# Kernel optimization log

Measured on AMD Instinct MI355X. Metric: run time of the kernel, lower is better.

Reference implementation:

```python
import jax, jax.numpy as jnp
import numpy as np

B, C, L = 4, 512, 4096

def setup_inputs() -> dict:
    key = jax.random.key(0)
    k1, k2, k3, k4 = jax.random.split(key, 4)
    proj_query = jax.random.normal(k1, (B, C, L), dtype=jnp.float32)
    proj_key = jax.random.normal(k2, (B, C, L), dtype=jnp.float32)
    proj_val = jax.random.normal(k3, (B, C, L), dtype=jnp.float32)
    # binary padding mask over key positions, broadcast over query axis
    padding_mask = (jax.random.uniform(k4, (B, 1, L)) < 0.9).astype(jnp.float32)
    return {"proj_query": proj_query, "proj_key": proj_key,
            "proj_val": proj_val, "padding_mask": padding_mask}

def reference(proj_query, proj_key, proj_val, padding_mask):
    c = proj_query.shape[1]
    # energy[b,i,j] = sum_c Q[b,c,i] * K[b,c,j]  -> (B, L1, L2)
    energy = jnp.einsum('bci,bcj->bij', proj_query, proj_key)
    attention = energy / jnp.sqrt(jnp.asarray(c, dtype=energy.dtype))
    attention = attention + jnp.log(padding_mask + 1e-6)
    attention = jax.nn.softmax(attention, axis=-1)
    attention = attention * padding_mask
    attention = attention.transpose(0, 2, 1)  # (B, L2, L1)
    out = jnp.einsum('bcj,bji->bci', proj_val, attention)  # (B, C, L1)
    return out, attention
```

## Files before the change

kernel.cpp:

```cpp
#include <hip/hip_runtime.h>

#define B_ 4
#define C_ 512
#define L_ 4096

typedef __attribute__((ext_vector_type(8))) short bf16x8;
typedef __attribute__((ext_vector_type(4))) float f32x4;

#define MFMA16(a, b, c) __builtin_amdgcn_mfma_f32_16x16x32_bf16(a, b, c, 0, 0, 0)

static __device__ __forceinline__ unsigned short f2bf_rne(float f) {
  unsigned u = __float_as_uint(f);
  u += 0x7FFFu + ((u >> 16) & 1u);
  return (unsigned short)(u >> 16);
}
static __device__ __forceinline__ unsigned pack_rne(float a, float b) {
  return (unsigned)f2bf_rne(a) | ((unsigned)f2bf_rne(b) << 16);
}
static __device__ __forceinline__ float bflo2f(unsigned w) {
  return __uint_as_float(w << 16);
}
static __device__ __forceinline__ float bfhi2f(unsigned w) {
  return __uint_as_float(w & 0xFFFF0000u);
}

static __device__ __forceinline__ void g2lds16(const unsigned short* g,
                                               unsigned short* l) {
  __builtin_amdgcn_global_load_lds(
      (const __attribute__((address_space(1))) unsigned int*)g,
      (__attribute__((address_space(3))) unsigned int*)l, 16, 0, 0);
}

#define BAR_() __builtin_amdgcn_s_barrier()
#define LGKM0_() asm volatile("s_waitcnt lgkmcnt(0)" ::: "memory")
#define VMW_(N) asm volatile("s_waitcnt vmcnt(" #N ")" ::: "memory")

__global__ __launch_bounds__(256) void prep_k(
    const float* __restrict__ Q, const float* __restrict__ K,
    const float* __restrict__ V, const float* __restrict__ mask,
    unsigned short* __restrict__ Qt, unsigned short* __restrict__ Kt,
    unsigned short* __restrict__ Vb) {
  int zb = blockIdx.z;
  int t = threadIdx.x;
  __shared__ float tile[64][65];
  if (zb < 8) {
    int b = zb >> 1;
    const float* src = ((zb & 1) ? K : Q) + (size_t)b * C_ * L_;
    unsigned short* dst = ((zb & 1) ? Kt : Qt) + (size_t)b * L_ * C_;
    int i0 = blockIdx.x * 64, c0 = blockIdx.y * 64;
    int cr = t >> 2, ig = (t & 3) * 16;
    const float* s = src + (size_t)(c0 + cr) * L_ + i0 + ig;
#pragma unroll
    for (int q = 0; q < 4; ++q) {
      float4 v = *(const float4*)(s + 4 * q);
      tile[cr][ig + 4 * q + 0] = v.x;
      tile[cr][ig + 4 * q + 1] = v.y;
      tile[cr][ig + 4 * q + 2] = v.z;
      tile[cr][ig + 4 * q + 3] = v.w;
    }
    __syncthreads();
    int ir = t >> 2, cg = (t & 3) * 16;
    unsigned wds[8];
#pragma unroll
    for (int k = 0; k < 8; ++k)
      wds[k] = pack_rne(tile[cg + 2 * k][ir], tile[cg + 2 * k + 1][ir]);
    unsigned short* d = dst + (size_t)(i0 + ir) * C_ + c0 + cg;
    uint4 o0, o1;
    o0.x = wds[0]; o0.y = wds[1]; o0.z = wds[2]; o0.w = wds[3];
    o1.x = wds[4]; o1.y = wds[5]; o1.z = wds[6]; o1.w = wds[7];
    *(uint4*)d = o0;
    *(uint4*)(d + 8) = o1;
  } else {
    int b = zb - 8;
    int flat = blockIdx.x + (blockIdx.y << 6);
    size_t base = (size_t)b * C_ * L_ + (size_t)flat * 4096 + (size_t)t * 16;
    int j = (int)(base & (L_ - 1));
    const float* vp = V + base;
    const float* mp = mask + (size_t)b * L_ + j;
#pragma unroll
    for (int g = 0; g < 2; ++g) {
      float4 v0 = *(const float4*)(vp + g * 8);
      float4 v1 = *(const float4*)(vp + g * 8 + 4);
      float4 m0 = *(const float4*)(mp + g * 8);
      float4 m1 = *(const float4*)(mp + g * 8 + 4);
      uint4 o;
      o.x = pack_rne(v0.x * m0.x, v0.y * m0.y);
      o.y = pack_rne(v0.z * m0.z, v0.w * m0.w);
      o.z = pack_rne(v1.x * m1.x, v1.y * m1.y);
      o.w = pack_rne(v1.z * m1.z, v1.w * m1.w);
      *(uint4*)(Vb + base + g * 8) = o;
    }
  }
}

__device__ __forceinline__ void gemm_8phase(
    const unsigned short* __restrict__ Ab,
    const unsigned short* __restrict__ Bb, int lda, int ldb, int Kdim,
    unsigned short* sA, unsigned short* sB, f32x4 (&acc)[8][4]) {
  const int t = threadIdx.x;
  const int lane = t & 63;
  const int quad = lane >> 4;
  const int l15 = lane & 15;
  const int w = t >> 6;
  const int wm = (w & 1) * 128;
  const int wn = (w >> 1) * 64;
  const int et = (t * 8) ^ (((t >> 5) & 1) << 4);
  const int srw = et >> 5;
  const int scl = et & 31;
  const int nt = Kdim >> 6;

  auto stage = [&](int nom, int hh) {
    int st = nom < nt ? nom : nt - 1;
    int db = nom & 1;
    int h = hh & 1;
    const unsigned short* g;
    unsigned short* l;
    if (hh < 2) {
      g = Bb + (size_t)(h * 128 + srw) * ldb + st * 64 + scl;
      l = sB + db * 16384 + h * 4096 + t * 8;
    } else {
      g = Ab + (size_t)(h * 128 + srw) * lda + st * 64 + scl;
      l = sA + db * 16384 + h * 4096 + t * 8;
    }
    g2lds16(g, l);
    g2lds16(g + 32, l + 8192);
  };
  auto rd = [&](const unsigned short* s, int db, int kc, int row) -> bf16x8 {
    int e = db * 16384 + kc * 8192 + row * 32 + quad * 8;
    e ^= ((e >> 8) & 1) << 4;
    return *(const bf16x8*)(s + e);
  };

  bf16x8 aF[4][2], b0[2][2], b1[2][2];
  auto rdA4 = [&](int db, int mbase) {
#pragma unroll
    for (int m = 0; m < 4; ++m)
#pragma unroll
      for (int kc = 0; kc < 2; ++kc)
        aF[m][kc] = rd(sA, db, kc, wm + (mbase + m) * 16 + l15);
  };
  auto rdB2 = [&](bf16x8 (&bf)[2][2], int db, int nbase) {
#pragma unroll
    for (int n = 0; n < 2; ++n)
#pragma unroll
      for (int kc = 0; kc < 2; ++kc)
        bf[n][kc] = rd(sB, db, kc, wn + (nbase + n) * 16 + l15);
  };
  auto mfma8 = [&](bf16x8 (&bf)[2][2], int mo, int no) {
    __builtin_amdgcn_s_setprio(1);
#pragma unroll
    for (int m = 0; m < 4; ++m)
#pragma unroll
      for (int n = 0; n < 2; ++n) {
        acc[mo + m][no + n] = MFMA16(aF[m][0], bf[n][0], acc[mo + m][no + n]);
        acc[mo + m][no + n] = MFMA16(aF[m][1], bf[n][1], acc[mo + m][no + n]);
      }
    __builtin_amdgcn_s_setprio(0);
  };

  stage(0, 0); stage(0, 1); stage(0, 2); stage(0, 3);
  asm volatile("s_waitcnt vmcnt(4)" ::: "memory");
  stage(1, 0); stage(1, 1); stage(1, 2);
  asm volatile("s_waitcnt vmcnt(6)" ::: "memory");
  BAR_();

  const int ni = nt >> 1;
  for (int i = 0; i < ni; ++i) {
    const int X = 2 * i;
    rdA4(0, 0); rdB2(b0, 0, 0); rdB2(b1, 0, 2);
    stage(X + 1, 3);
    BAR_(); LGKM0_();
    mfma8(b0, 0, 0);
    BAR_();
    stage(X + 2, 0);
    BAR_();
    mfma8(b1, 0, 2);
    BAR_();
    rdA4(0, 4);
    stage(X + 2, 1);
    BAR_(); LGKM0_();
    mfma8(b0, 4, 0);
    BAR_();
    stage(X + 2, 2);
    VMW_(6); BAR_();
    mfma8(b1, 4, 2);
    BAR_(); __builtin_amdgcn_sched_barrier(0);
    rdA4(1, 0); rdB2(b0, 1, 0); rdB2(b1, 1, 2);
    stage(X + 2, 3);
    BAR_(); LGKM0_();
    mfma8(b0, 0, 0);
    BAR_();
    stage(X + 3, 0);
    BAR_();
    mfma8(b1, 0, 2);
    BAR_();
    rdA4(1, 4);
    stage(X + 3, 1);
    BAR_(); LGKM0_();
    mfma8(b0, 4, 0);
    BAR_();
    stage(X + 3, 2);
    VMW_(6); BAR_();
    mfma8(b1, 4, 2);
    BAR_(); __builtin_amdgcn_sched_barrier(0);
  }
  asm volatile("s_waitcnt vmcnt(0)" ::: "memory");
}

__global__ __launch_bounds__(512, 2) void gemm1_8p_k(
    const unsigned short* __restrict__ Qt, const unsigned short* __restrict__ Kt,
    const float* __restrict__ mask, unsigned short* __restrict__ t0,
    unsigned short* __restrict__ t1, unsigned short* __restrict__ t2,
    unsigned short* __restrict__ t3, float* __restrict__ rowsum) {
  __shared__ unsigned short sA[32768];
  __shared__ unsigned short sB[32768];
  int flat = blockIdx.x + (blockIdx.y << 4) + (blockIdx.z << 8);
  int swz = (flat & 7) * 128 + (flat >> 3);
  int bx = swz & 15, by = (swz >> 4) & 15, b = swz >> 8;
  unsigned short* tbb = (b == 0) ? t0 : (b == 1) ? t1 : (b == 2) ? t2 : t3;
  int i0 = by * 256, j0 = bx * 256;
  f32x4 acc[8][4] = {};
  gemm_8phase(Qt + (size_t)b * L_ * C_ + (size_t)i0 * C_,
              Kt + (size_t)b * L_ * C_ + (size_t)j0 * C_, C_, C_, C_, sA, sB,
              acc);
  int t = threadIdx.x;
  int lane = t & 63;
  int quad = lane >> 4;
  int l15 = lane & 15;
  int w = t >> 6;
  int wm = (w & 1) * 128;
  int wn = (w >> 1) * 64;
  const float scale = 0.04419417382415922f;
  float lm[4], mv[4];
#pragma unroll
  for (int n = 0; n < 4; ++n) {
    int j = j0 + wn + n * 16 + l15;
    float m = mask[(size_t)b * L_ + j];
    mv[n] = m;
    lm[n] = __logf(m + 1e-6f);
  }
  float rs[8][4];
#pragma unroll
  for (int m = 0; m < 8; ++m)
#pragma unroll
    for (int r = 0; r < 4; ++r) rs[m][r] = 0.f;
#pragma unroll
  for (int m = 0; m < 8; ++m) {
    int irow = i0 + wm + m * 16 + quad * 4;
#pragma unroll
    for (int r = 0; r < 4; ++r) {
      size_t ro = (size_t)(irow + r) * L_;
#pragma unroll
      for (int n = 0; n < 4; ++n) {
        float x = fminf(acc[m][n][r] * scale + lm[n], 60.f);
        float tv = __expf(x);
        rs[m][r] += tv;
        tbb[ro + j0 + wn + n * 16 + l15] = f2bf_rne(tv * mv[n]);
      }
    }
  }
#pragma unroll
  for (int mm = 1; mm < 16; mm <<= 1)
#pragma unroll
    for (int m = 0; m < 8; ++m)
#pragma unroll
      for (int r = 0; r < 4; ++r) rs[m][r] += __shfl_xor(rs[m][r], mm, 64);
  if (l15 == 0) {
    float* rb = rowsum + (size_t)b * L_ + i0 + wm;
#pragma unroll
    for (int m = 0; m < 8; ++m)
#pragma unroll
      for (int r = 0; r < 4; ++r)
        atomicAdd(&rb[m * 16 + quad * 4 + r], rs[m][r]);
  }
}

__global__ __launch_bounds__(512, 2) void gemm2_8p_k(
    const unsigned short* __restrict__ Vb, const unsigned short* __restrict__ t0,
    const unsigned short* __restrict__ t1, const unsigned short* __restrict__ t2,
    const unsigned short* __restrict__ t3, const float* __restrict__ rowsum,
    float* __restrict__ out, float* __restrict__ out2) {
  __shared__ unsigned short sA[32768];
  __shared__ unsigned short sB[32768];
  int flat = blockIdx.x + (blockIdx.y << 4) + (blockIdx.z << 5);
  int swz = (flat & 7) * 32 + (flat >> 3);
  int ix = swz & 15, cy = (swz >> 4) & 1, z = swz >> 5;
  int b = z & 3, ks = z >> 2;
  const unsigned short* tbb =
      (b == 0) ? t0 : (b == 1) ? t1 : (b == 2) ? t2 : t3;
  int i0 = ix * 256, c0 = cy * 256;
  f32x4 acc[8][4] = {};
  gemm_8phase(Vb + (size_t)b * C_ * L_ + (size_t)c0 * L_ + ks * (L_ / 2),
              tbb + (size_t)i0 * L_ + ks * (L_ / 2), L_, L_, L_ / 2, sA, sB,
              acc);
  int t = threadIdx.x;
  int lane = t & 63;
  int quad = lane >> 4;
  int l15 = lane & 15;
  int w = t >> 6;
  int wm = (w & 1) * 128;
  int wn = (w >> 1) * 64;
  float invv[4];
#pragma unroll
  for (int n = 0; n < 4; ++n)
    invv[n] = 1.0f / rowsum[(size_t)b * L_ + i0 + wn + n * 16 + l15];
  float* ob = (ks ? out2 : out) + (size_t)b * C_ * L_;
#pragma unroll
  for (int m = 0; m < 8; ++m) {
    int crow = c0 + wm + m * 16 + quad * 4;
#pragma unroll
    for (int r = 0; r < 4; ++r) {
      size_t ro = (size_t)(crow + r) * L_;
#pragma unroll
      for (int n = 0; n < 4; ++n)
        ob[ro + i0 + wn + n * 16 + l15] = acc[m][n][r] * invv[n];
    }
  }
}

__global__ __launch_bounds__(256) void finalize_all_k(
    const unsigned short* __restrict__ tb, const float* __restrict__ rowsum,
    float* __restrict__ attn, float* __restrict__ out,
    const float* __restrict__ out2) {
  int b = blockIdx.z;
  int t = threadIdx.x;
  if (out2 != nullptr) {
    int flat = blockIdx.x + (blockIdx.y << 6) + (blockIdx.z << 12);
    if (flat < 8192) {
      size_t idx = (size_t)flat * 1024 + (size_t)t * 4;
      float4 a = *(const float4*)(out + idx);
      float4 c = *(const float4*)(out2 + idx);
      a.x += c.x; a.y += c.y; a.z += c.z; a.w += c.w;
      *(float4*)(out + idx) = a;
    }
  }
  const unsigned short* src = tb + (size_t)b * L_ * L_;
  const float* rs = rowsum + (size_t)b * L_;
  float* dst = attn + (size_t)b * L_ * L_;
  int jt = blockIdx.x, it = blockIdx.y;
  __shared__ float tileT[64][65];
  int r = t >> 2, cg = (t & 3) * 16;
  int i = it * 64 + r;
  float inv = 1.0f / rs[i];
  const unsigned short* sp = src + (size_t)i * L_ + jt * 64 + cg;
  uint4 u0 = *(const uint4*)sp;
  uint4 u1 = *(const uint4*)(sp + 8);
  const unsigned* w0 = (const unsigned*)&u0;
  const unsigned* w1 = (const unsigned*)&u1;
#pragma unroll
  for (int k = 0; k < 4; ++k) {
    tileT[cg + 2 * k + 0][r] = bflo2f(w0[k]) * inv;
    tileT[cg + 2 * k + 1][r] = bfhi2f(w0[k]) * inv;
    tileT[cg + 8 + 2 * k + 0][r] = bflo2f(w1[k]) * inv;
    tileT[cg + 8 + 2 * k + 1][r] = bfhi2f(w1[k]) * inv;
  }
  __syncthreads();
  float* dp = dst + (size_t)(jt * 64 + r) * L_ + it * 64 + cg;
#pragma unroll
  for (int q = 0; q < 4; ++q) {
    float4 o;
    o.x = tileT[r][cg + 4 * q + 0];
    o.y = tileT[r][cg + 4 * q + 1];
    o.z = tileT[r][cg + 4 * q + 2];
    o.w = tileT[r][cg + 4 * q + 3];
    *(float4*)(dp + 4 * q) = o;
  }
}

__device__ __forceinline__ void gemm_mainloop64(
    const unsigned short* Ab, const unsigned short* Bb, int lda, int ldb,
    int Kdim, unsigned short* sA, unsigned short* sB, f32x4 acc[4][4]) {
  int t = threadIdx.x;
  const unsigned short* pA[4];
  const unsigned short* pB[4];
#pragma unroll
  for (int c = 0; c < 4; ++c) {
    int e = t * 8 + c * 2048;
    int kc = e >> 12;
    int rem = e & 4095;
    int row = rem >> 5;
    int col = rem & 31;
    int off = kc * 32 + col;
    pA[c] = Ab + (size_t)row * lda + off;
    pB[c] = Bb + (size_t)row * ldb + off;
  }
  int lane = t & 63;
  int quad = lane >> 4;
  int l15 = lane & 15;
  int w = t >> 6;
  int wm = (w & 1) * 64;
  int wn = (w >> 1) * 64;
  for (int kk = 0; kk < Kdim; kk += 64) {
    __syncthreads();
#pragma unroll
    for (int c = 0; c < 4; ++c) g2lds16(pA[c] + kk, sA + t * 8 + c * 2048);
#pragma unroll
    for (int c = 0; c < 4; ++c) g2lds16(pB[c] + kk, sB + t * 8 + c * 2048);
    __syncthreads();
#pragma unroll
    for (int kc = 0; kc < 2; ++kc) {
      bf16x8 aF[4], bF[4];
#pragma unroll
      for (int ti = 0; ti < 4; ++ti)
        aF[ti] = *(const bf16x8*)(sA + kc * 4096 +
                                  (wm + ti * 16 + l15) * 32 + quad * 8);
#pragma unroll
      for (int tj = 0; tj < 4; ++tj)
        bF[tj] = *(const bf16x8*)(sB + kc * 4096 +
                                  (wn + tj * 16 + l15) * 32 + quad * 8);
#pragma unroll
      for (int ti = 0; ti < 4; ++ti)
#pragma unroll
        for (int tj = 0; tj < 4; ++tj)
          acc[ti][tj] = MFMA16(aF[ti], bF[tj], acc[ti][tj]);
    }
  }
}

__global__ __launch_bounds__(256) void gemm1_bf_k(
    const unsigned short* __restrict__ Qt, const unsigned short* __restrict__ Kt,
    const float* __restrict__ mask, unsigned short* __restrict__ t0,
    unsigned short* __restrict__ t1, unsigned short* __restrict__ t2,
    unsigned short* __restrict__ t3, float* __restrict__ rowsum) {
  int b = blockIdx.z;
  unsigned short* tbb = (b == 0) ? t0 : (b == 1) ? t1 : (b == 2) ? t2 : t3;
  int i0 = blockIdx.y * 128;
  int j0 = blockIdx.x * 128;
  __shared__ unsigned short sA[8192];
  __shared__ unsigned short sB[8192];
  f32x4 acc[4][4] = {};
  gemm_mainloop64(Qt + (size_t)b * L_ * C_ + (size_t)i0 * C_,
                  Kt + (size_t)b * L_ * C_ + (size_t)j0 * C_, C_, C_, C_, sA,
                  sB, acc);
  int t = threadIdx.x;
  int lane = t & 63;
  int quad = lane >> 4;
  int l15 = lane & 15;
  int w = t >> 6;
  int wm = (w & 1) * 64;
  int wn = (w >> 1) * 64;
  const float scale = 0.04419417382415922f;
  float lm[4], mv[4];
#pragma unroll
  for (int tj = 0; tj < 4; ++tj) {
    int j = j0 + wn + tj * 16 + l15;
    float m = mask[(size_t)b * L_ + j];
    mv[tj] = m;
    lm[tj] = __logf(m + 1e-6f);
  }
  float rs[16];
#pragma unroll
  for (int q = 0; q < 16; ++q) rs[q] = 0.f;
#pragma unroll
  for (int ti = 0; ti < 4; ++ti) {
    int irow = i0 + wm + ti * 16 + quad * 4;
#pragma unroll
    for (int r = 0; r < 4; ++r) {
      size_t ro = (size_t)(irow + r) * L_;
#pragma unroll
      for (int tj = 0; tj < 4; ++tj) {
        float x = fminf(acc[ti][tj][r] * scale + lm[tj], 60.f);
        float tv = __expf(x);
        rs[ti * 4 + r] += tv;
        tbb[ro + j0 + wn + tj * 16 + l15] = f2bf_rne(tv * mv[tj]);
      }
    }
  }
#pragma unroll
  for (int m = 1; m < 16; m <<= 1)
#pragma unroll
    for (int q = 0; q < 16; ++q) rs[q] += __shfl_xor(rs[q], m, 64);
  if (l15 == 0) {
    float* rb = rowsum + (size_t)b * L_ + i0 + wm;
#pragma unroll
    for (int ti = 0; ti < 4; ++ti)
#pragma unroll
      for (int r = 0; r < 4; ++r)
        atomicAdd(&rb[ti * 16 + quad * 4 + r], rs[ti * 4 + r]);
  }
}

__global__ __launch_bounds__(256) void gemm2_bf_k(
    const unsigned short* __restrict__ Vb, const unsigned short* __restrict__ t0,
    const unsigned short* __restrict__ t1, const unsigned short* __restrict__ t2,
    const unsigned short* __restrict__ t3, const float* __restrict__ rowsum,
    float* __restrict__ out) {
  int z = blockIdx.z;
  int b = z & 3;
  int ks = z >> 2;
  const unsigned short* tbb =
      (b == 0) ? t0 : (b == 1) ? t1 : (b == 2) ? t2 : t3;
  int c0 = blockIdx.y * 128;
  int i0 = blockIdx.x * 128;
  __shared__ unsigned short sA[8192];
  __shared__ unsigned short sB[8192];
  f32x4 acc[4][4] = {};
  gemm_mainloop64(Vb + (size_t)b * C_ * L_ + (size_t)c0 * L_ + ks * (L_ / 2),
                  tbb + (size_t)i0 * L_ + ks * (L_ / 2), L_, L_, L_ / 2, sA, sB,
                  acc);
  int t = threadIdx.x;
  int lane = t & 63;
  int quad = lane >> 4;
  int l15 = lane & 15;
  int w = t >> 6;
  int wm = (w & 1) * 64;
  int wn = (w >> 1) * 64;
  float invv[4];
#pragma unroll
  for (int tj = 0; tj < 4; ++tj)
    invv[tj] = 1.0f / rowsum[(size_t)b * L_ + i0 + wn + tj * 16 + l15];
  float* ob = out + (size_t)b * C_ * L_;
#pragma unroll
  for (int ti = 0; ti < 4; ++ti) {
    int crow = c0 + wm + ti * 16 + quad * 4;
#pragma unroll
    for (int r = 0; r < 4; ++r) {
      size_t ro = (size_t)(crow + r) * L_;
#pragma unroll
      for (int tj = 0; tj < 4; ++tj)
        atomicAdd(&ob[ro + i0 + wn + tj * 16 + l15],
                  acc[ti][tj][r] * invv[tj]);
    }
  }
}

extern "C" void kernel_launch(void* const* d_in, const int* in_sizes, int n_in,
                              void* d_out, int out_size, void* d_ws,
                              size_t ws_size, hipStream_t stream) {
  const float* Q = (const float*)d_in[0];
  const float* K = (const float*)d_in[1];
  const float* V = (const float*)d_in[2];
  const float* mask = (const float*)d_in[3];

  float* out = (float*)d_out;
  float* attn = out + (size_t)B_ * C_ * L_;

  const size_t NQ = (size_t)B_ * L_ * C_;
  const size_t SLOT = (size_t)L_ * L_;
  unsigned short* Qt = (unsigned short*)d_ws;
  unsigned short* Kt = Qt + NQ;
  unsigned short* Vb = Kt + NQ;
  float* rowsum = (float*)(Vb + NQ);
  unsigned short* wtail = (unsigned short*)(rowsum + (size_t)B_ * L_);

  const size_t need1 =
      NQ * 2 * 3 + (size_t)B_ * L_ * 4 + (size_t)B_ * SLOT * 2 + NQ * 4;

  hipMemsetAsync(rowsum, 0, (size_t)B_ * L_ * sizeof(float), stream);
  prep_k<<<dim3(64, 8, 12), 256, 0, stream>>>(Q, K, V, mask, Qt, Kt, Vb);

  if (ws_size >= need1) {
    unsigned short* tb = wtail;
    float* out2 = (float*)(tb + (size_t)B_ * SLOT);
    gemm1_8p_k<<<dim3(16, 16, B_), 512, 0, stream>>>(
        Qt, Kt, mask, tb, tb + SLOT, tb + 2 * SLOT, tb + 3 * SLOT, rowsum);
    gemm2_8p_k<<<dim3(16, 2, B_ * 2), 512, 0, stream>>>(
        Vb, tb, tb + SLOT, tb + 2 * SLOT, tb + 3 * SLOT, rowsum, out, out2);
    finalize_all_k<<<dim3(64, 64, B_), 256, 0, stream>>>(tb, rowsum, attn, out,
                                                         out2);
  } else {
    unsigned short* tb0 = (unsigned short*)(attn + 2 * SLOT);
    unsigned short* tb1 = (unsigned short*)(attn + 3 * SLOT);
    unsigned short* tb2 = (unsigned short*)(attn + 3 * SLOT + SLOT / 2);
    unsigned short* tb3 = wtail;
    hipMemsetAsync(out, 0, (size_t)B_ * C_ * L_ * sizeof(float), stream);
    gemm1_bf_k<<<dim3(L_ / 128, L_ / 128, B_), 256, 0, stream>>>(
        Qt, Kt, mask, tb0, tb1, tb2, tb3, rowsum);
    gemm2_bf_k<<<dim3(L_ / 128, C_ / 128, B_ * 2), 256, 0, stream>>>(
        Vb, tb0, tb1, tb2, tb3, rowsum, out);
    finalize_all_k<<<dim3(64, 64, 1), 256, 0, stream>>>(tb0, rowsum, attn,
                                                        nullptr, nullptr);
    finalize_all_k<<<dim3(64, 64, 1), 256, 0, stream>>>(tb1, rowsum + L_,
                                                        attn + SLOT, nullptr,
                                                        nullptr);
    finalize_all_k<<<dim3(64, 64, 1), 256, 0, stream>>>(tb2, rowsum + 2 * L_,
                                                        attn + 2 * SLOT,
                                                        nullptr, nullptr);
    finalize_all_k<<<dim3(64, 64, 1), 256, 0, stream>>>(tb3, rowsum + 3 * L_,
                                                        attn + 3 * SLOT,
                                                        nullptr, nullptr);
  }
}
```

Measured before the change: 654.2 us.

## Replace 8-phase 256x256 GEMM with simple double-buffered 128x128 tiles

Replaces the hand-scheduled 8-phase 256x256-tile GEMM (512 threads, two blocks per CU) with a simpler double-buffered 128x128-tile GEMM on 256 threads, for both the QK^T and the PV kernels. Grids become 1D with an XCD-aware block swizzle. The rowsum zeroing moves from a separate memset into the prep kernel, saving one launch. Smaller tiles raise block count and may improve occupancy, but they lower data reuse and drop the fine-grained interleave of loads with MFMA, since each step waits on vmcnt(0).

```diff
diff --git a/kernel.cpp b/kernel.cpp
--- a/kernel.cpp
+++ b/kernel.cpp
@@ -32,14 +32,13 @@
 }
 
 #define BAR_() __builtin_amdgcn_s_barrier()
-#define LGKM0_() asm volatile("s_waitcnt lgkmcnt(0)" ::: "memory")
-#define VMW_(N) asm volatile("s_waitcnt vmcnt(" #N ")" ::: "memory")
+#define VMW0_() asm volatile("s_waitcnt vmcnt(0)" ::: "memory")
 
 __global__ __launch_bounds__(256) void prep_k(
     const float* __restrict__ Q, const float* __restrict__ K,
     const float* __restrict__ V, const float* __restrict__ mask,
     unsigned short* __restrict__ Qt, unsigned short* __restrict__ Kt,
-    unsigned short* __restrict__ Vb) {
+    unsigned short* __restrict__ Vb, float* __restrict__ rowsum) {
   int zb = blockIdx.z;
   int t = threadIdx.x;
   __shared__ float tile[64][65];
@@ -73,6 +72,12 @@
   } else {
     int b = zb - 8;
     int flat = blockIdx.x + (blockIdx.y << 6);
+    if (b == 0 && flat == 0) {
+      float4 z4 = {0.f, 0.f, 0.f, 0.f};
+#pragma unroll
+      for (int q = 0; q < 16; ++q)
+        *(float4*)(rowsum + (q * 256 + t) * 4) = z4;
+    }
     size_t base = (size_t)b * C_ * L_ + (size_t)flat * 4096 + (size_t)t * 16;
     int j = (int)(base & (L_ - 1));
     const float* vp = V + base;
@@ -93,227 +98,179 @@
   }
 }
 
-__device__ __forceinline__ void gemm_8phase(
+__device__ __forceinline__ void gemm_dbuf(
     const unsigned short* __restrict__ Ab,
     const unsigned short* __restrict__ Bb, int lda, int ldb, int Kdim,
-    unsigned short* sA, unsigned short* sB, f32x4 (&acc)[8][4]) {
+    unsigned short* sA, unsigned short* sB, f32x4 (&acc)[4][4]) {
   const int t = threadIdx.x;
   const int lane = t & 63;
   const int quad = lane >> 4;
   const int l15 = lane & 15;
   const int w = t >> 6;
-  const int wm = (w & 1) * 128;
+  const int wm = (w & 1) * 64;
   const int wn = (w >> 1) * 64;
-  const int et = (t * 8) ^ (((t >> 5) & 1) << 4);
-  const int srw = et >> 5;
-  const int scl = et & 31;
-  const int nt = Kdim >> 6;
-
-  auto stage = [&](int nom, int hh) {
-    int st = nom < nt ? nom : nt - 1;
+  const int sw = ((t >> 5) & 1) << 4;
+  const int ntt = Kdim >> 6;
+
+  auto stage = [&](int nom) {
+    int kk = nom * 64;
     int db = nom & 1;
-    int h = hh & 1;
-    const unsigned short* g;
-    unsigned short* l;
-    if (hh < 2) {
-      g = Bb + (size_t)(h * 128 + srw) * ldb + st * 64 + scl;
-      l = sB + db * 16384 + h * 4096 + t * 8;
-    } else {
-      g = Ab + (size_t)(h * 128 + srw) * lda + st * 64 + scl;
-      l = sA + db * 16384 + h * 4096 + t * 8;
-    }
-    g2lds16(g, l);
-    g2lds16(g + 32, l + 8192);
+#pragma unroll
+    for (int c = 0; c < 4; ++c) {
+      int e = (t * 8 + c * 2048) ^ sw;
+      int kc = e >> 12;
+      int row = (e & 4095) >> 5;
+      int col = e & 31;
+      int go = kk + kc * 32 + col;
+      unsigned short* la = sA + db * 8192 + t * 8 + c * 2048;
+      unsigned short* lb = sB + db * 8192 + t * 8 + c * 2048;
+      g2lds16(Ab + (size_t)row * lda + go, la);
+      g2lds16(Bb + (size_t)row * ldb + go, lb);
+    }
   };
   auto rd = [&](const unsigned short* s, int db, int kc, int row) -> bf16x8 {
-    int e = db * 16384 + kc * 8192 + row * 32 + quad * 8;
+    int e = kc * 4096 + row * 32 + quad * 8;
     e ^= ((e >> 8) & 1) << 4;
-    return *(const bf16x8*)(s + e);
+    return *(const bf16x8*)(s + db * 8192 + e);
   };
 
-  bf16x8 aF[4][2], b0[2][2], b1[2][2];
-  auto rdA4 = [&](int db, int mbase) {
+  stage(0);
+  for (int kt = 0; kt < ntt; ++kt) {
+    int db = kt & 1;
+    VMW0_();
+    BAR_();
+    if (kt + 1 < ntt) stage(kt + 1);
+    bf16x8 aF[4][2], bF[4][2];
 #pragma unroll
     for (int m = 0; m < 4; ++m)
 #pragma unroll
       for (int kc = 0; kc < 2; ++kc)
-        aF[m][kc] = rd(sA, db, kc, wm + (mbase + m) * 16 + l15);
-  };
-  auto rdB2 = [&](bf16x8 (&bf)[2][2], int db, int nbase) {
-#pragma unroll
-    for (int n = 0; n < 2; ++n)
+        aF[m][kc] = rd(sA, db, kc, wm + m * 16 + l15);
+#pragma unroll
+    for (int n = 0; n < 4; ++n)
 #pragma unroll
       for (int kc = 0; kc < 2; ++kc)
-        bf[n][kc] = rd(sB, db, kc, wn + (nbase + n) * 16 + l15);
-  };
-  auto mfma8 = [&](bf16x8 (&bf)[2][2], int mo, int no) {
+        bF[n][kc] = rd(sB, db, kc, wn + n * 16 + l15);
     __builtin_amdgcn_s_setprio(1);
 #pragma unroll
     for (int m = 0; m < 4; ++m)
 #pragma unroll
-      for (int n = 0; n < 2; ++n) {
-        acc[mo + m][no + n] = MFMA16(aF[m][0], bf[n][0], acc[mo + m][no + n]);
-        acc[mo + m][no + n] = MFMA16(aF[m][1], bf[n][1], acc[mo + m][no + n]);
+      for (int n = 0; n < 4; ++n) {
+        acc[m][n] = MFMA16(aF[m][0], bF[n][0], acc[m][n]);
+        acc[m][n] = MFMA16(aF[m][1], bF[n][1], acc[m][n]);
       }
     __builtin_amdgcn_s_setprio(0);
-  };
-
-  stage(0, 0); stage(0, 1); stage(0, 2); stage(0, 3);
-  asm volatile("s_waitcnt vmcnt(4)" ::: "memory");
-  stage(1, 0); stage(1, 1); stage(1, 2);
-  asm volatile("s_waitcnt vmcnt(6)" ::: "memory");
-  BAR_();
-
-  const int ni = nt >> 1;
-  for (int i = 0; i < ni; ++i) {
-    const int X = 2 * i;
-    rdA4(0, 0); rdB2(b0, 0, 0); rdB2(b1, 0, 2);
-    stage(X + 1, 3);
-    BAR_(); LGKM0_();
-    mfma8(b0, 0, 0);
-    BAR_();
-    stage(X + 2, 0);
-    BAR_();
-    mfma8(b1, 0, 2);
-    BAR_();
-    rdA4(0, 4);
-    stage(X + 2, 1);
-    BAR_(); LGKM0_();
-    mfma8(b0, 4, 0);
-    BAR_();
-    stage(X + 2, 2);
-    VMW_(6); BAR_();
-    mfma8(b1, 4, 2);
-    BAR_(); __builtin_amdgcn_sched_barrier(0);
-    rdA4(1, 0); rdB2(b0, 1, 0); rdB2(b1, 1, 2);
-    stage(X + 2, 3);
-    BAR_(); LGKM0_();
-    mfma8(b0, 0, 0);
-    BAR_();
-    stage(X + 3, 0);
-    BAR_();
-    mfma8(b1, 0, 2);
-    BAR_();
-    rdA4(1, 4);
-    stage(X + 3, 1);
-    BAR_(); LGKM0_();
-    mfma8(b0, 4, 0);
-    BAR_();
-    stage(X + 3, 2);
-    VMW_(6); BAR_();
-    mfma8(b1, 4, 2);
-    BAR_(); __builtin_amdgcn_sched_barrier(0);
-  }
-  asm volatile("s_waitcnt vmcnt(0)" ::: "memory");
-}
-
-__global__ __launch_bounds__(512, 2) void gemm1_8p_k(
+  }
+}
+
+__global__ __launch_bounds__(256) void gemm1_db_k(
     const unsigned short* __restrict__ Qt, const unsigned short* __restrict__ Kt,
     const float* __restrict__ mask, unsigned short* __restrict__ t0,
     unsigned short* __restrict__ t1, unsigned short* __restrict__ t2,
     unsigned short* __restrict__ t3, float* __restrict__ rowsum) {
-  __shared__ unsigned short sA[32768];
-  __shared__ unsigned short sB[32768];
-  int flat = blockIdx.x + (blockIdx.y << 4) + (blockIdx.z << 8);
-  int swz = (flat & 7) * 128 + (flat >> 3);
-  int bx = swz & 15, by = (swz >> 4) & 15, b = swz >> 8;
+  __shared__ unsigned short sA[16384];
+  __shared__ unsigned short sB[16384];
+  int f = blockIdx.x;
+  int g = f & 7;
+  int s = f >> 3;
+  int b = g >> 1;
+  int bx = (s & 15) + ((g & 1) << 4);
+  int by = s >> 4;
   unsigned short* tbb = (b == 0) ? t0 : (b == 1) ? t1 : (b == 2) ? t2 : t3;
-  int i0 = by * 256, j0 = bx * 256;
-  f32x4 acc[8][4] = {};
-  gemm_8phase(Qt + (size_t)b * L_ * C_ + (size_t)i0 * C_,
-              Kt + (size_t)b * L_ * C_ + (size_t)j0 * C_, C_, C_, C_, sA, sB,
-              acc);
+  int i0 = by * 128, j0 = bx * 128;
+  f32x4 acc[4][4] = {};
+  gemm_dbuf(Qt + (size_t)b * L_ * C_ + (size_t)i0 * C_,
+            Kt + (size_t)b * L_ * C_ + (size_t)j0 * C_, C_, C_, C_, sA, sB,
+            acc);
   int t = threadIdx.x;
   int lane = t & 63;
   int quad = lane >> 4;
   int l15 = lane & 15;
   int w = t >> 6;
-  int wm = (w & 1) * 128;
+  int wm = (w & 1) * 64;
   int wn = (w >> 1) * 64;
   const float scale = 0.04419417382415922f;
   float lm[4], mv[4];
 #pragma unroll
-  for (int n = 0; n < 4; ++n) {
-    int j = j0 + wn + n * 16 + l15;
+  for (int tj = 0; tj < 4; ++tj) {
+    int j = j0 + wn + tj * 16 + l15;
     float m = mask[(size_t)b * L_ + j];
-    mv[n] = m;
-    lm[n] = __logf(m + 1e-6f);
-  }
-  float rs[8][4];
-#pragma unroll
-  for (int m = 0; m < 8; ++m)
-#pragma unroll
-    for (int r = 0; r < 4; ++r) rs[m][r] = 0.f;
-#pragma unroll
-  for (int m = 0; m < 8; ++m) {
-    int irow = i0 + wm + m * 16 + quad * 4;
+    mv[tj] = m;
+    lm[tj] = __logf(m + 1e-6f);
+  }
+  float rs[16];
+#pragma unroll
+  for (int q = 0; q < 16; ++q) rs[q] = 0.f;
+#pragma unroll
+  for (int ti = 0; ti < 4; ++ti) {
+    int irow = i0 + wm + ti * 16 + quad * 4;
 #pragma unroll
     for (int r = 0; r < 4; ++r) {
       size_t ro = (size_t)(irow + r) * L_;
 #pragma unroll
-      for (int n = 0; n < 4; ++n) {
-        float x = fminf(acc[m][n][r] * scale + lm[n], 60.f);
+      for (int tj = 0; tj < 4; ++tj) {
+        float x = fminf(acc[ti][tj][r] * scale + lm[tj], 60.f);
         float tv = __expf(x);
-        rs[m][r] += tv;
-        tbb[ro + j0 + wn + n * 16 + l15] = f2bf_rne(tv * mv[n]);
+        rs[ti * 4 + r] += tv;
+        tbb[ro + j0 + wn + tj * 16 + l15] = f2bf_rne(tv * mv[tj]);
       }
     }
   }
 #pragma unroll
-  for (int mm = 1; mm < 16; mm <<= 1)
-#pragma unroll
-    for (int m = 0; m < 8; ++m)
-#pragma unroll
-      for (int r = 0; r < 4; ++r) rs[m][r] += __shfl_xor(rs[m][r], mm, 64);
+  for (int m = 1; m < 16; m <<= 1)
+#pragma unroll
+    for (int q = 0; q < 16; ++q) rs[q] += __shfl_xor(rs[q], m, 64);
   if (l15 == 0) {
     float* rb = rowsum + (size_t)b * L_ + i0 + wm;
 #pragma unroll
-    for (int m = 0; m < 8; ++m)
+    for (int ti = 0; ti < 4; ++ti)
 #pragma unroll
       for (int r = 0; r < 4; ++r)
-        atomicAdd(&rb[m * 16 + quad * 4 + r], rs[m][r]);
-  }
-}
-
-__global__ __launch_bounds__(512, 2) void gemm2_8p_k(
+        atomicAdd(&rb[ti * 16 + quad * 4 + r], rs[ti * 4 + r]);
+  }
+}
+
+__global__ __launch_bounds__(256) void gemm2_db_k(
     const unsigned short* __restrict__ Vb, const unsigned short* __restrict__ t0,
     const unsigned short* __restrict__ t1, const unsigned short* __restrict__ t2,
     const unsigned short* __restrict__ t3, const float* __restrict__ rowsum,
     float* __restrict__ out, float* __restrict__ out2) {
-  __shared__ unsigned short sA[32768];
-  __shared__ unsigned short sB[32768];
-  int flat = blockIdx.x + (blockIdx.y << 4) + (blockIdx.z << 5);
-  int swz = (flat & 7) * 32 + (flat >> 3);
-  int ix = swz & 15, cy = (swz >> 4) & 1, z = swz >> 5;
-  int b = z & 3, ks = z >> 2;
+  __shared__ unsigned short sA[16384];
+  __shared__ unsigned short sB[16384];
+  int f = blockIdx.x;
+  int g = f & 7;
+  int s = f >> 3;
+  int b = g & 3, ks = g >> 2;
+  int cy = s & 3;
+  int ix = s >> 2;
   const unsigned short* tbb =
       (b == 0) ? t0 : (b == 1) ? t1 : (b == 2) ? t2 : t3;
-  int i0 = ix * 256, c0 = cy * 256;
-  f32x4 acc[8][4] = {};
-  gemm_8phase(Vb + (size_t)b * C_ * L_ + (size_t)c0 * L_ + ks * (L_ / 2),
-              tbb + (size_t)i0 * L_ + ks * (L_ / 2), L_, L_, L_ / 2, sA, sB,
-              acc);
+  int i0 = ix * 128, c0 = cy * 128;
+  f32x4 acc[4][4] = {};
+  gemm_dbuf(Vb + (size_t)b * C_ * L_ + (size_t)c0 * L_ + ks * (L_ / 2),
+            tbb + (size_t)i0 * L_ + ks * (L_ / 2), L_, L_, L_ / 2, sA, sB,
+            acc);
   int t = threadIdx.x;
   int lane = t & 63;
   int quad = lane >> 4;
   int l15 = lane & 15;
   int w = t >> 6;
-  int wm = (w & 1) * 128;
+  int wm = (w & 1) * 64;
   int wn = (w >> 1) * 64;
   float invv[4];
 #pragma unroll
-  for (int n = 0; n < 4; ++n)
-    invv[n] = 1.0f / rowsum[(size_t)b * L_ + i0 + wn + n * 16 + l15];
+  for (int tj = 0; tj < 4; ++tj)
+    invv[tj] = 1.0f / rowsum[(size_t)b * L_ + i0 + wn + tj * 16 + l15];
   float* ob = (ks ? out2 : out) + (size_t)b * C_ * L_;
 #pragma unroll
-  for (int m = 0; m < 8; ++m) {
-    int crow = c0 + wm + m * 16 + quad * 4;
+  for (int ti = 0; ti < 4; ++ti) {
+    int crow = c0 + wm + ti * 16 + quad * 4;
 #pragma unroll
     for (int r = 0; r < 4; ++r) {
       size_t ro = (size_t)(crow + r) * L_;
 #pragma unroll
-      for (int n = 0; n < 4; ++n)
-        ob[ro + i0 + wn + n * 16 + l15] = acc[m][n][r] * invv[n];
+      for (int tj = 0; tj < 4; ++tj)
+        ob[ro + i0 + wn + tj * 16 + l15] = acc[ti][tj][r] * invv[tj];
     }
   }
 }
@@ -546,15 +503,15 @@
   const size_t need1 =
       NQ * 2 * 3 + (size_t)B_ * L_ * 4 + (size_t)B_ * SLOT * 2 + NQ * 4;
 
-  hipMemsetAsync(rowsum, 0, (size_t)B_ * L_ * sizeof(float), stream);
-  prep_k<<<dim3(64, 8, 12), 256, 0, stream>>>(Q, K, V, mask, Qt, Kt, Vb);
+  prep_k<<<dim3(64, 8, 12), 256, 0, stream>>>(Q, K, V, mask, Qt, Kt, Vb,
+                                              rowsum);
 
   if (ws_size >= need1) {
     unsigned short* tb = wtail;
     float* out2 = (float*)(tb + (size_t)B_ * SLOT);
-    gemm1_8p_k<<<dim3(16, 16, B_), 512, 0, stream>>>(
+    gemm1_db_k<<<dim3(4096), 256, 0, stream>>>(
         Qt, Kt, mask, tb, tb + SLOT, tb + 2 * SLOT, tb + 3 * SLOT, rowsum);
-    gemm2_8p_k<<<dim3(16, 2, B_ * 2), 512, 0, stream>>>(
+    gemm2_db_k<<<dim3(1024), 256, 0, stream>>>(
         Vb, tb, tb + SLOT, tb + 2 * SLOT, tb + 3 * SLOT, rowsum, out, out2);
     finalize_all_k<<<dim3(64, 64, B_), 256, 0, stream>>>(tb, rowsum, attn, out,
                                                          out2);
```

Measured after the change: 682.3 us. 4.3% more time.

## Replace LDS-staged gemm1 with direct-load 128x128 tiles; fold rowsum zeroing into prep

Applied to the files above, without the earlier changes.

The first QK^T GEMM drops the 256x256 LDS-staged 8-phase pipeline. It becomes a 128x128-tile kernel that loads bf16 fragments straight from global memory into registers, double-buffered across k steps, launched as 4096 blocks of 256 threads with a grouped block ordering. The aim is higher occupancy and no LDS or barrier overhead, at the cost of less data reuse and more global and L2 traffic per FLOP. The rowsum memset moves into the prep kernel to save a launch. It also changes the column computation in the fallback mainloop, which may alter that path's addressing.

```diff
diff --git a/kernel.cpp b/kernel.cpp
--- a/kernel.cpp
+++ b/kernel.cpp
@@ -39,7 +39,7 @@
     const float* __restrict__ Q, const float* __restrict__ K,
     const float* __restrict__ V, const float* __restrict__ mask,
     unsigned short* __restrict__ Qt, unsigned short* __restrict__ Kt,
-    unsigned short* __restrict__ Vb) {
+    unsigned short* __restrict__ Vb, float* __restrict__ rowsum) {
   int zb = blockIdx.z;
   int t = threadIdx.x;
   __shared__ float tile[64][65];
@@ -73,6 +73,12 @@
   } else {
     int b = zb - 8;
     int flat = blockIdx.x + (blockIdx.y << 6);
+    if (b == 0 && flat == 0) {
+      float4 z4 = {0.f, 0.f, 0.f, 0.f};
+#pragma unroll
+      for (int q = 0; q < 16; ++q)
+        *(float4*)(rowsum + (q * 256 + t) * 4) = z4;
+    }
     size_t base = (size_t)b * C_ * L_ + (size_t)flat * 4096 + (size_t)t * 16;
     int j = (int)(base & (L_ - 1));
     const float* vp = V + base;
@@ -90,6 +96,105 @@
       o.w = pack_rne(v1.z * m1.z, v1.w * m1.w);
       *(uint4*)(Vb + base + g * 8) = o;
     }
+  }
+}
+
+__global__ __launch_bounds__(256, 3) void gemm1_nl_k(
+    const unsigned short* __restrict__ Qt, const unsigned short* __restrict__ Kt,
+    const float* __restrict__ mask, unsigned short* __restrict__ t0,
+    unsigned short* __restrict__ t1, unsigned short* __restrict__ t2,
+    unsigned short* __restrict__ t3, float* __restrict__ rowsum) {
+  int f = blockIdx.x;
+  int g = f & 7;
+  int s = f >> 3;
+  int b = g >> 1;
+  int bx = (s & 15) + ((g & 1) << 4);
+  int by = s >> 4;
+  unsigned short* tbb = (b == 0) ? t0 : (b == 1) ? t1 : (b == 2) ? t2 : t3;
+  int i0 = by * 128, j0 = bx * 128;
+  const unsigned short* Ab = Qt + (size_t)b * L_ * C_ + (size_t)i0 * C_;
+  const unsigned short* Bb = Kt + (size_t)b * L_ * C_ + (size_t)j0 * C_;
+
+  int t = threadIdx.x;
+  int lane = t & 63;
+  int quad = lane >> 4;
+  int l15 = lane & 15;
+  int w = t >> 6;
+  int wm = (w & 1) * 64;
+  int wn = (w >> 1) * 64;
+
+  const unsigned short* pa[4];
+  const unsigned short* pb[4];
+#pragma unroll
+  for (int m = 0; m < 4; ++m)
+    pa[m] = Ab + (size_t)(wm + m * 16 + l15) * C_ + quad * 8;
+#pragma unroll
+  for (int n = 0; n < 4; ++n)
+    pb[n] = Bb + (size_t)(wn + n * 16 + l15) * C_ + quad * 8;
+
+  f32x4 acc[4][4] = {};
+  bf16x8 a0[4], b0[4], a1[4], b1[4];
+
+  auto ldf = [&](bf16x8 (&aa)[4], bf16x8 (&bb)[4], int kk) {
+#pragma unroll
+    for (int m = 0; m < 4; ++m) aa[m] = *(const bf16x8*)(pa[m] + kk);
+#pragma unroll
+    for (int n = 0; n < 4; ++n) bb[n] = *(const bf16x8*)(pb[n] + kk);
+  };
+  auto mm = [&](bf16x8 (&aa)[4], bf16x8 (&bb)[4]) {
+#pragma unroll
+    for (int m = 0; m < 4; ++m)
+#pragma unroll
+      for (int n = 0; n < 4; ++n)
+        acc[m][n] = MFMA16(aa[m], bb[n], acc[m][n]);
+  };
+
+  ldf(a0, b0, 0);
+  for (int kk = 0; kk < C_; kk += 64) {
+    ldf(a1, b1, kk + 32);
+    mm(a0, b0);
+    if (kk + 64 < C_) ldf(a0, b0, kk + 64);
+    mm(a1, b1);
+  }
+
+  const float scale = 0.04419417382415922f;
+  float lm[4], mv[4];
+#pragma unroll
+  for (int tj = 0; tj < 4; ++tj) {
+    int j = j0 + wn + tj * 16 + l15;
+    float m = mask[(size_t)b * L_ + j];
+    mv[tj] = m;
+    lm[tj] = __logf(m + 1e-6f);
+  }
+  float rs[16];
+#pragma unroll
+  for (int q = 0; q < 16; ++q) rs[q] = 0.f;
+#pragma unroll
+  for (int ti = 0; ti < 4; ++ti) {
+    int irow = i0 + wm + ti * 16 + quad * 4;
+#pragma unroll
+    for (int r = 0; r < 4; ++r) {
+      size_t ro = (size_t)(irow + r) * L_;
+#pragma unroll
+      for (int tj = 0; tj < 4; ++tj) {
+        float x = fminf(acc[ti][tj][r] * scale + lm[tj], 60.f);
+        float tv = __expf(x);
+        rs[ti * 4 + r] += tv;
+        tbb[ro + j0 + wn + tj * 16 + l15] = f2bf_rne(tv * mv[tj]);
+      }
+    }
+  }
+#pragma unroll
+  for (int m = 1; m < 16; m <<= 1)
+#pragma unroll
+    for (int q = 0; q < 16; ++q) rs[q] += __shfl_xor(rs[q], m, 64);
+  if (l15 == 0) {
+    float* rb = rowsum + (size_t)b * L_ + i0 + wm;
+#pragma unroll
+    for (int ti = 0; ti < 4; ++ti)
+#pragma unroll
+      for (int r = 0; r < 4; ++r)
+        atomicAdd(&rb[ti * 16 + quad * 4 + r], rs[ti * 4 + r]);
   }
 }
 
@@ -205,74 +310,6 @@
     BAR_(); __builtin_amdgcn_sched_barrier(0);
   }
   asm volatile("s_waitcnt vmcnt(0)" ::: "memory");
-}
-
-__global__ __launch_bounds__(512, 2) void gemm1_8p_k(
-    const unsigned short* __restrict__ Qt, const unsigned short* __restrict__ Kt,
-    const float* __restrict__ mask, unsigned short* __restrict__ t0,
-    unsigned short* __restrict__ t1, unsigned short* __restrict__ t2,
-    unsigned short* __restrict__ t3, float* __restrict__ rowsum) {
-  __shared__ unsigned short sA[32768];
-  __shared__ unsigned short sB[32768];
-  int flat = blockIdx.x + (blockIdx.y << 4) + (blockIdx.z << 8);
-  int swz = (flat & 7) * 128 + (flat >> 3);
-  int bx = swz & 15, by = (swz >> 4) & 15, b = swz >> 8;
-  unsigned short* tbb = (b == 0) ? t0 : (b == 1) ? t1 : (b == 2) ? t2 : t3;
-  int i0 = by * 256, j0 = bx * 256;
-  f32x4 acc[8][4] = {};
-  gemm_8phase(Qt + (size_t)b * L_ * C_ + (size_t)i0 * C_,
-              Kt + (size_t)b * L_ * C_ + (size_t)j0 * C_, C_, C_, C_, sA, sB,
-              acc);
-  int t = threadIdx.x;
-  int lane = t & 63;
-  int quad = lane >> 4;
-  int l15 = lane & 15;
-  int w = t >> 6;
-  int wm = (w & 1) * 128;
-  int wn = (w >> 1) * 64;
-  const float scale = 0.04419417382415922f;
-  float lm[4], mv[4];
-#pragma unroll
-  for (int n = 0; n < 4; ++n) {
-    int j = j0 + wn + n * 16 + l15;
-    float m = mask[(size_t)b * L_ + j];
-    mv[n] = m;
-    lm[n] = __logf(m + 1e-6f);
-  }
-  float rs[8][4];
-#pragma unroll
-  for (int m = 0; m < 8; ++m)
-#pragma unroll
-    for (int r = 0; r < 4; ++r) rs[m][r] = 0.f;
-#pragma unroll
-  for (int m = 0; m < 8; ++m) {
-    int irow = i0 + wm + m * 16 + quad * 4;
-#pragma unroll
-    for (int r = 0; r < 4; ++r) {
-      size_t ro = (size_t)(irow + r) * L_;
-#pragma unroll
-      for (int n = 0; n < 4; ++n) {
-        float x = fminf(acc[m][n][r] * scale + lm[n], 60.f);
-        float tv = __expf(x);
-        rs[m][r] += tv;
-        tbb[ro + j0 + wn + n * 16 + l15] = f2bf_rne(tv * mv[n]);
-      }
-    }
-  }
-#pragma unroll
-  for (int mm = 1; mm < 16; mm <<= 1)
-#pragma unroll
-    for (int m = 0; m < 8; ++m)
-#pragma unroll
-      for (int r = 0; r < 4; ++r) rs[m][r] += __shfl_xor(rs[m][r], mm, 64);
-  if (l15 == 0) {
-    float* rb = rowsum + (size_t)b * L_ + i0 + wm;
-#pragma unroll
-    for (int m = 0; m < 8; ++m)
-#pragma unroll
-      for (int r = 0; r < 4; ++r)
-        atomicAdd(&rb[m * 16 + quad * 4 + r], rs[m][r]);
-  }
 }
 
 __global__ __launch_bounds__(512, 2) void gemm2_8p_k(
@@ -379,7 +416,7 @@
     int kc = e >> 12;
     int rem = e & 4095;
     int row = rem >> 5;
-    int col = rem & 31;
+    int col = e & 31;
     int off = kc * 32 + col;
     pA[c] = Ab + (size_t)row * lda + off;
     pB[c] = Bb + (size_t)row * ldb + off;
@@ -546,13 +583,13 @@
   const size_t need1 =
       NQ * 2 * 3 + (size_t)B_ * L_ * 4 + (size_t)B_ * SLOT * 2 + NQ * 4;
 
-  hipMemsetAsync(rowsum, 0, (size_t)B_ * L_ * sizeof(float), stream);
-  prep_k<<<dim3(64, 8, 12), 256, 0, stream>>>(Q, K, V, mask, Qt, Kt, Vb);
+  prep_k<<<dim3(64, 8, 12), 256, 0, stream>>>(Q, K, V, mask, Qt, Kt, Vb,
+                                              rowsum);
 
   if (ws_size >= need1) {
     unsigned short* tb = wtail;
     float* out2 = (float*)(tb + (size_t)B_ * SLOT);
-    gemm1_8p_k<<<dim3(16, 16, B_), 512, 0, stream>>>(
+    gemm1_nl_k<<<dim3(4096), 256, 0, stream>>>(
         Qt, Kt, mask, tb, tb + SLOT, tb + 2 * SLOT, tb + 3 * SLOT, rowsum);
     gemm2_8p_k<<<dim3(16, 2, B_ * 2), 512, 0, stream>>>(
         Vb, tb, tb + SLOT, tb + 2 * SLOT, tb + 3 * SLOT, rowsum, out, out2);
```

After: 791.5 us. +21.0%, slower.
